# Performance work log

Hardware: AMD Instinct MI355X
Metric: run time of the kernel (lower is better)

## Reference

```python
import jax, jax.numpy as jnp
import numpy as np

N = 100000      # num nodes
E = 400000      # num edges (avg degree 4, AIG-like sparse DAG)
NVT = 7         # node type count (one-hot)
VHS = 100       # vertex hidden size
CHS = 30        # clause hidden size
SV = 512        # number of state-variable nodes
NROUNDS = 8     # message passing rounds


def setup_inputs() -> dict:
    key = jax.random.key(0)
    ks = jax.random.split(key, 40)
    s = 0.08  # ~1/sqrt(VHS), matches torch default uniform scale

    def mat(k, shape):
        return jax.random.normal(k, shape, jnp.float32) * s

    edge_index = jax.random.randint(ks[0], (2, E), 0, N)
    sv_node = jax.random.randint(ks[1], (SV,), 0, N)
    types = jax.random.randint(ks[2], (N,), 0, NVT)
    x = jax.nn.one_hot(types, NVT, dtype=jnp.float32)  # [N, NVT]
    ones_e = jnp.ones((E,), jnp.float32)
    # degrees used as divisors after SpMM (clamped >= 1 like real graphs w/ self edges)
    ind = jnp.clip(jax.ops.segment_sum(ones_e, edge_index[1], num_segments=N), 1.0, None)
    outd = jnp.clip(jax.ops.segment_sum(ones_e, edge_index[0], num_segments=N), 1.0, None)

    inp = {
        "x": x, "edge_index": edge_index, "sv_node": sv_node,
        "ind": ind, "outd": outd, "n_clause": 1, "pretrain_round": 1,
        # type init vectors: Linear(1,VHS)(ones(1)) == weight[:,0] + bias, one row per type
        "type_vec": mat(ks[3], (NVT, VHS)),
        # forward_msg MLP
        "fm_w1": mat(ks[4], (VHS, VHS)), "fm_b1": mat(ks[5], (VHS,)),
        "fm_w2": mat(ks[6], (VHS, VHS)), "fm_b2": mat(ks[7], (VHS,)),
        "fm_w3": mat(ks[8], (VHS, VHS)), "fm_b3": mat(ks[9], (VHS,)),
        # backward_msg MLP
        "bm_w1": mat(ks[10], (VHS, VHS)), "bm_b1": mat(ks[11], (VHS,)),
        "bm_w2": mat(ks[12], (VHS, VHS)), "bm_b2": mat(ks[13], (VHS,)),
        "bm_w3": mat(ks[14], (VHS, VHS)), "bm_b3": mat(ks[15], (VHS,)),
        # forward_update GRU (gates ordered r,z,n as in torch)
        "fg_wih": mat(ks[16], (VHS, 3 * VHS)), "fg_whh": mat(ks[17], (VHS, 3 * VHS)),
        "fg_bih": mat(ks[18], (3 * VHS,)), "fg_bhh": mat(ks[19], (3 * VHS,)),
        # backward_update GRU
        "bg_wih": mat(ks[20], (VHS, 3 * VHS)), "bg_whh": mat(ks[21], (VHS, 3 * VHS)),
        "bg_bih": mat(ks[22], (3 * VHS,)), "bg_bhh": mat(ks[23], (3 * VHS,)),
        # sv_feature_pretrain_layer
        "pw1": mat(ks[24], (VHS, CHS)), "pb1": mat(ks[25], (CHS,)),
        "pw2": mat(ks[26], (CHS, 1)), "pb2": mat(ks[27], (1,)),
    }
    return inp


def reference(x, edge_index, sv_node, ind, outd, n_clause, pretrain_round,
              type_vec, fm_w1, fm_b1, fm_w2, fm_b2, fm_w3, fm_b3,
              bm_w1, bm_b1, bm_w2, bm_b2, bm_w3, bm_b3,
              fg_wih, fg_whh, fg_bih, fg_bhh,
              bg_wih, bg_whh, bg_bih, bg_bhh,
              pw1, pb1, pw2, pb2):
    n = x.shape[0]
    src, dst = edge_index[0], edge_index[1]
    ind_c = ind[:, None]   # [N,1]
    outd_c = outd[:, None]

    def mlp(h, w1, b1, w2, b2, w3, b3):
        h = jax.nn.relu(h @ w1 + b1)
        h = jax.nn.relu(h @ w2 + b2)
        return h @ w3 + b3

    def gru(xin, h, wih, whh, bih, bhh):
        # single-step torch GRU: r,z,n gate ordering
        gi = xin @ wih + bih
        gh = h @ whh + bhh
        ir, iz, ig = jnp.split(gi, 3, axis=-1)
        hr, hz, hg = jnp.split(gh, 3, axis=-1)
        r = jax.nn.sigmoid(ir + hr)
        z = jax.nn.sigmoid(iz + hz)
        g = jnp.tanh(ig + r * hg)
        return (1.0 - z) * g + z * h

    def round_fn(vs, _):
        # forward direction: adj_fwd[dst, src] -> aggregate msgs from src into dst
        m = mlp(vs, fm_w1, fm_b1, fm_w2, fm_b2, fm_w3, fm_b3)
        fwd = jax.ops.segment_sum(m[src], dst, num_segments=n) / ind_c
        vs = gru(fwd, vs, fg_wih, fg_whh, fg_bih, fg_bhh)
        # backward direction: adj_bwd[src, dst] -> aggregate msgs from dst into src
        m = mlp(vs, bm_w1, bm_b1, bm_w2, bm_b2, bm_w3, bm_b3)
        bwd = jax.ops.segment_sum(m[dst], src, num_segments=n) / outd_c
        vs = gru(bwd, vs, bg_wih, bg_whh, bg_bih, bg_bhh)
        return vs, None

    vs0 = x @ type_vec  # [N, VHS]
    vs, _ = jax.lax.scan(jax.checkpoint(round_fn), vs0, None, length=NROUNDS)

    # pretrain_round branch: sv_feature_pretrain_layer(var_state[sv_node]).t()[0]
    shortcut = vs[sv_node]  # [SV, VHS]
    h = jax.nn.relu(shortcut @ pw1 + pb1)
    return (h @ pw2 + pb2)[:, 0]  # [SV]
```

## Files before the change

### kernel.cpp

```cpp
#include <hip/hip_runtime.h>
#include <math.h>

#define NVTC 7
#define VHS 100
#define CHS 30
#define LDP 112
#define CTW 128
#define WFRAG_SZ 32768

typedef short short8 __attribute__((ext_vector_type(8)));
typedef float floatx4 __attribute__((ext_vector_type(4)));

#define MFMA(a, b, c) __builtin_amdgcn_mfma_f32_16x16x32_bf16((a), (b), (c), 0, 0, 0)

#define GLOAD16(g, l)                                                              \
  __builtin_amdgcn_global_load_lds((const __attribute__((address_space(1))) void*)(g), \
                                   (__attribute__((address_space(3))) void*)(l), 16, 0, 0)

__device__ __forceinline__ unsigned short f2bf(float f) {
  unsigned u = __float_as_uint(f);
  return (unsigned short)((u + 0x7fffu + ((u >> 16) & 1u)) >> 16);
}
__device__ __forceinline__ float bf2f(unsigned short h) {
  return __uint_as_float((unsigned)h << 16);
}
__device__ __forceinline__ float sigmf(float v) {
  return __builtin_amdgcn_rcpf(1.f + __expf(-v));
}
__device__ __forceinline__ float tanh_fast(float v) {
  return 1.f - 2.f * __builtin_amdgcn_rcpf(__expf(2.f * v) + 1.f);
}


__global__ void zero_int_kernel(int* __restrict__ p, int n) {
  int i = blockIdx.x * 256 + threadIdx.x;
  if (i < n) p[i] = 0;
}

__global__ void inv_kernel(const float* __restrict__ ind, const float* __restrict__ outd,
                           float* __restrict__ inv_ind, float* __restrict__ inv_outd, int n) {
  int i = blockIdx.x * 256 + threadIdx.x;
  if (i < n) { inv_ind[i] = 1.0f / ind[i]; inv_outd[i] = 1.0f / outd[i]; }
}

struct WfragArgs { const float* src; int srcLD; int colOff; short* dst; };
struct WfragPack { WfragArgs a[18]; };
__global__ void wfrag_all_kernel(WfragPack p) {
  const int mat = blockIdx.x >> 3;
  const int t = ((blockIdx.x & 7) << 8) + threadIdx.x;
  const WfragArgs w = p.a[mat];
  int lane = t & 63, rest = t >> 6;
  int ct = rest & 7, kc = rest >> 3;
  int col = ct * 16 + (lane & 15);
  int kbase = kc * 32 + (lane >> 4) * 8;
  short8 hv, lv;
  #pragma unroll
  for (int i = 0; i < 8; ++i) {
    int k = kbase + i;
    float v = (k < VHS && col < VHS) ? w.src[(size_t)k * w.srcLD + w.colOff + col] : 0.f;
    unsigned short h16 = f2bf(v);
    hv[i] = (short)h16;
    lv[i] = (short)f2bf(v - bf2f(h16));
  }
  int base = ((kc * 8 + ct) * 2 * 64 + lane) * 8;
  *(short8*)(w.dst + base)       = hv;
  *(short8*)(w.dst + base + 512) = lv;
}

struct PadArgs { const float* b1; int off1; const float* b2; int off2; float* dst; };
struct PadPack { PadArgs a[14]; };
__global__ void pad_all_kernel(PadPack p) {
  const PadArgs w = p.a[blockIdx.x];
  int c = threadIdx.x;
  float v = 0.f;
  if (c < VHS) { v = w.b1[w.off1 + c]; if (w.b2) v += w.b2[w.off2 + c]; }
  w.dst[c] = v;
}

__global__ void init_vs_kernel(const float* __restrict__ x, const float* __restrict__ tv,
                               char* __restrict__ vsp, int N) {
  int node = blockIdx.x, c = threadIdx.x;
  if (node >= N) return;
  float v = 0.f;
  if (c < VHS) {
    #pragma unroll
    for (int t = 0; t < NVTC; ++t) v += x[(size_t)node * NVTC + t] * tv[t * VHS + c];
  }
  unsigned short hi = f2bf(v);
  unsigned short lo = f2bf(v - bf2f(hi));
  char* rowp = vsp + ((size_t)node << 9);
  *(unsigned short*)(rowp + 2 * c)       = hi;
  *(unsigned short*)(rowp + 256 + 2 * c) = lo;
}


__global__ void hist_kernel(const int* __restrict__ ei, int E, int* hin, int* hout) {
  int e = blockIdx.x * 256 + threadIdx.x;
  if (e < E) {
    atomicAdd(&hout[ei[e]], 1);
    atomicAdd(&hin[ei[E + e]], 1);
  }
}

__global__ void scan_block_kernel(const int* __restrict__ in, int* __restrict__ mid,
                                  int* __restrict__ sums, int n) {
  __shared__ int lds[256];
  int tid = threadIdx.x;
  int base = blockIdx.x * 1024 + tid * 4;
  int v0 = (base + 0 < n) ? in[base + 0] : 0;
  int v1 = (base + 1 < n) ? in[base + 1] : 0;
  int v2 = (base + 2 < n) ? in[base + 2] : 0;
  int v3 = (base + 3 < n) ? in[base + 3] : 0;
  int s = v0 + v1 + v2 + v3;
  lds[tid] = s;
  __syncthreads();
  for (int off = 1; off < 256; off <<= 1) {
    int t = (tid >= off) ? lds[tid - off] : 0;
    __syncthreads();
    lds[tid] += t;
    __syncthreads();
  }
  int excl = lds[tid] - s;
  int e0 = excl + v0, e1 = e0 + v1, e2 = e1 + v2, e3 = e2 + v3;
  if (base + 0 < n) mid[base + 0] = e0;
  if (base + 1 < n) mid[base + 1] = e1;
  if (base + 2 < n) mid[base + 2] = e2;
  if (base + 3 < n) mid[base + 3] = e3;
  if (tid == 255) sums[blockIdx.x] = lds[255];
}

__global__ void scan_sums_kernel(int* sums, int nb) {
  __shared__ int lds[256];
  int tid = threadIdx.x;
  int v = (tid < nb) ? sums[tid] : 0;
  lds[tid] = v;
  __syncthreads();
  for (int off = 1; off < 256; off <<= 1) {
    int t = (tid >= off) ? lds[tid - off] : 0;
    __syncthreads();
    lds[tid] += t;
    __syncthreads();
  }
  if (tid < nb) sums[tid] = lds[tid];
}

__global__ void scan_finalize_kernel(const int* __restrict__ mid, const int* __restrict__ sums,
                                     int* __restrict__ rp, int n) {
  int i = blockIdx.x * 256 + threadIdx.x;
  if (i >= n) return;
  int blk = i >> 10;
  int add = (blk > 0) ? sums[blk - 1] : 0;
  rp[i + 1] = mid[i] + add;
  if (i == 0) rp[0] = 0;
}

__global__ void fill_kernel(const int* __restrict__ ei, int E, int gOff, int sOff,
                            const int* __restrict__ rp, int* cnt, int* col) {
  int e = blockIdx.x * 256 + threadIdx.x;
  if (e >= E) return;
  int v = ei[sOff + e];
  int p = rp[v] + atomicAdd(&cnt[v], 1);
  col[p] = ei[gOff + e];
}

__global__ void sort_rows_kernel(const int* __restrict__ rp, int* col, int n) {
  int v = blockIdx.x * 256 + threadIdx.x;
  if (v >= n) return;
  int a = rp[v], b = rp[v + 1];
  for (int i = a + 1; i < b; ++i) {
    int key = col[i];
    int j = i - 1;
    while (j >= a && col[j] > key) { col[j + 1] = col[j]; --j; }
    col[j + 1] = key;
  }
}

__global__ void __launch_bounds__(256)
gather_kernel(const float* __restrict__ m, const int* __restrict__ rp,
              const int* __restrict__ col, const float* __restrict__ iv,
              char* __restrict__ aggp, int N) {
  int v = blockIdx.x * 8 + (threadIdx.x >> 5);
  if (v >= N) return;
  int lane = threadIdx.x & 31;
  char* rowp = aggp + ((size_t)v << 9);
  if (lane < 28) {
    float4 a = make_float4(0.f, 0.f, 0.f, 0.f);
    float4 b = make_float4(0.f, 0.f, 0.f, 0.f);
    const int s = rp[v], e = rp[v + 1];
    int i = s;
    for (; i + 1 < e; i += 2) {
      const int c0 = col[i], c1 = col[i + 1];
      float4 u = ((const float4*)(m + (size_t)c0 * LDP))[lane];
      float4 w = ((const float4*)(m + (size_t)c1 * LDP))[lane];
      a.x += u.x; a.y += u.y; a.z += u.z; a.w += u.w;
      b.x += w.x; b.y += w.y; b.z += w.z; b.w += w.w;
    }
    if (i < e) {
      float4 u = ((const float4*)(m + (size_t)col[i] * LDP))[lane];
      a.x += u.x; a.y += u.y; a.z += u.z; a.w += u.w;
    }
    a.x += b.x; a.y += b.y; a.z += b.z; a.w += b.w;
    const float sc = iv[v];
    a.x *= sc; a.y *= sc; a.z *= sc; a.w *= sc;
    unsigned short h0 = f2bf(a.x), h1 = f2bf(a.y), h2 = f2bf(a.z), h3 = f2bf(a.w);
    unsigned short l0 = f2bf(a.x - bf2f(h0)), l1 = f2bf(a.y - bf2f(h1));
    unsigned short l2 = f2bf(a.z - bf2f(h2)), l3 = f2bf(a.w - bf2f(h3));
    *(uint2*)(rowp + 8 * lane) =
        make_uint2((unsigned)h0 | ((unsigned)h1 << 16), (unsigned)h2 | ((unsigned)h3 << 16));
    *(uint2*)(rowp + 256 + 8 * lane) =
        make_uint2((unsigned)l0 | ((unsigned)l1 << 16), (unsigned)l2 | ((unsigned)l3 << 16));
  } else {
    *(uint2*)(rowp + 8 * lane)       = make_uint2(0u, 0u);
    *(uint2*)(rowp + 256 + 8 * lane) = make_uint2(0u, 0u);
  }
}

__global__ void __launch_bounds__(256, 2)
mlp3_kernel(const char* __restrict__ vsp,
            const short* __restrict__ W1f, const short* __restrict__ W2f,
            const short* __restrict__ W3f,
            const float* __restrict__ b1, const float* __restrict__ b2,
            const float* __restrict__ b3, float* __restrict__ OUT, int N) {
  __shared__ __align__(16) char lds[65536];
  char* ldsH = lds;
  char* ldsL = lds + 16384;
  const int lane = threadIdx.x & 63, wave = threadIdx.x >> 6;
  const int lrbase = wave * 16;
  const int row0 = blockIdx.x * 64 + lrbase;
  const int a_r = lane & 15, a_kg = lane >> 4;
  const int col_l = lane & 15;

  short8 Fh[4], Fl[4];
  {
    const char* vrow = vsp + (((size_t)(row0 + a_r)) << 9) + (a_kg << 4);
    #pragma unroll
    for (int kc = 0; kc < 4; ++kc) {
      Fh[kc] = *(const short8*)(vrow + kc * 64);
      Fl[kc] = *(const short8*)(vrow + 256 + kc * 64);
    }
  }
  float B1[7], B2[7], B3[7];
  #pragma unroll
  for (int ct = 0; ct < 7; ++ct) {
    const int k = ct * 16 + col_l;
    B1[ct] = b1[k]; B2[ct] = b2[k]; B3[ct] = b3[k];
  }
  if (lane < 32) {
    int row = lrbase + (lane >> 1), sl = 14 + (lane & 1);
    int byte = row * 256 + ((sl * 16) ^ ((row & 7) << 4));
    short8 z = {0, 0, 0, 0, 0, 0, 0, 0};
    *(short8*)(ldsH + byte) = z;
    *(short8*)(ldsL + byte) = z;
  }
  asm volatile("s_waitcnt vmcnt(0)" ::: "memory");

  floatx4 acc[7];
  #pragma unroll
  for (int c = 0; c < 7; ++c) acc[c] = (floatx4){0.f, 0.f, 0.f, 0.f};

#define MSTAGE(WF, KC, BOFF)                                                   \
  {                                                                            \
    _Pragma("unroll") for (int q = 0; q < 4; ++q) {                            \
      const int c_ = wave * 4 + q;                                             \
      GLOAD16((const char*)(WF) + (size_t)((KC) * 16384 + c_ * 1024) + lane * 16, \
              lds + (BOFF) + c_ * 1024);                                       \
    }                                                                          \
  }

#define MCOMP(KC, BOFF, VA)                                                    \
  {                                                                            \
    asm volatile("s_waitcnt vmcnt(" VA ")" ::: "memory");                      \
    __builtin_amdgcn_s_barrier();                                              \
    short8 wt[14];                                                             \
    _Pragma("unroll") for (int c = 0; c < 7; ++c) {                            \
      wt[2 * c]     = *(const short8*)(lds + (BOFF) + (2 * c) * 1024 + lane * 16); \
      wt[2 * c + 1] = *(const short8*)(lds + (BOFF) + (2 * c + 1) * 1024 + lane * 16); \
    }                                                                          \
    __builtin_amdgcn_s_setprio(1);                                             \
    _Pragma("unroll") for (int c = 0; c < 7; ++c) {                            \
      acc[c] = MFMA(Fh[KC], wt[2 * c], acc[c]);                                \
      acc[c] = MFMA(Fh[KC], wt[2 * c + 1], acc[c]);                            \
      acc[c] = MFMA(Fl[KC], wt[2 * c], acc[c]);                                \
    }                                                                          \
    __builtin_amdgcn_s_setprio(0);                                             \
    __builtin_amdgcn_sched_barrier(0);                                         \
    __builtin_amdgcn_s_barrier();                                              \
  }

  auto wbrelu = [&](const float* B) {
    const int rloc0 = lrbase + (lane >> 4) * 4;
    #pragma unroll
    for (int ct = 0; ct < 7; ++ct) {
      int k = ct * 16 + col_l;
      #pragma unroll
      for (int j = 0; j < 4; ++j) {
        int row = rloc0 + j;
        float v = fmaxf(acc[ct][j] + B[ct], 0.f);
        unsigned short h16 = f2bf(v);
        unsigned short l16 = f2bf(v - bf2f(h16));
        int byte = row * 256 + ((k * 2) ^ ((row & 7) << 4));
        *(short*)(ldsH + byte) = (short)h16;
        *(short*)(ldsL + byte) = (short)l16;
      }
      acc[ct] = (floatx4){0.f, 0.f, 0.f, 0.f};
    }
  };
  auto ldfrags = [&]() {
    #pragma unroll
    for (int kc = 0; kc < 4; ++kc) {
      int r = lrbase + a_r;
      int byte = r * 256 + ((((kc * 4 + a_kg) * 16)) ^ ((r & 7) << 4));
      Fh[kc] = *(const short8*)(ldsH + byte);
      Fl[kc] = *(const short8*)(ldsL + byte);
    }
  };

  MSTAGE(W1f, 0, 32768) MSTAGE(W1f, 1, 49152)
  MCOMP(0, 32768, "4")  MSTAGE(W1f, 2, 32768)
  MCOMP(1, 49152, "4")  MSTAGE(W1f, 3, 49152)
  MCOMP(2, 32768, "4")  MSTAGE(W2f, 0, 32768)
  MCOMP(3, 49152, "4")  MSTAGE(W2f, 1, 49152)
  wbrelu(B1); ldfrags();
  MCOMP(0, 32768, "4")  MSTAGE(W2f, 2, 32768)
  MCOMP(1, 49152, "4")  MSTAGE(W2f, 3, 49152)
  MCOMP(2, 32768, "4")  MSTAGE(W3f, 0, 32768)
  MCOMP(3, 49152, "4")  MSTAGE(W3f, 1, 49152)
  wbrelu(B2); ldfrags();
  MCOMP(0, 32768, "4")  MSTAGE(W3f, 2, 32768)
  MCOMP(1, 49152, "4")  MSTAGE(W3f, 3, 49152)
  MCOMP(2, 32768, "4")
  MCOMP(3, 49152, "0")

  const int r0 = row0 + (lane >> 4) * 4;
  #pragma unroll
  for (int ct = 0; ct < 7; ++ct) {
    const int c = ct * 16 + col_l;
    #pragma unroll
    for (int j = 0; j < 4; ++j) {
      const int r = r0 + j;
      if (r < N) OUT[(size_t)r * LDP + c] = acc[ct][j] + B3[ct];
    }
  }
#undef MSTAGE
#undef MCOMP
}

__global__ void __launch_bounds__(256, 2)
gru_kernel(const char* __restrict__ aggp, const char* __restrict__ vsp,
           const short* __restrict__ Wbase,
           const float* __restrict__ br, const float* __restrict__ bz,
           const float* __restrict__ big, const float* __restrict__ bhg,
           char* __restrict__ outp, int N) {
  __shared__ __align__(16) char wlds[49152];
  const int lane = threadIdx.x & 63, wave = threadIdx.x >> 6;
  const int row0 = blockIdx.x * 64 + wave * 16;
  const int a_r = lane & 15;
  const int kgo = (lane >> 4) << 4;
  const int col_l = lane & 15;
  const int jr0 = row0 + (lane >> 4) * 4;

  short8 Ah[4], Al[4], Vh[4], Vl[4];
  {
    const char* arow = aggp + (((size_t)(row0 + a_r)) << 9) + kgo;
    const char* vrow = vsp  + (((size_t)(row0 + a_r)) << 9) + kgo;
    #pragma unroll
    for (int kc = 0; kc < 4; ++kc) {
      Ah[kc] = *(const short8*)(arow + kc * 64);
      Al[kc] = *(const short8*)(arow + 256 + kc * 64);
      Vh[kc] = *(const short8*)(vrow + kc * 64);
      Vl[kc] = *(const short8*)(vrow + 256 + kc * 64);
    }
  }
  float ho[7][4];
  #pragma unroll
  for (int ct = 0; ct < 7; ++ct) {
    const int ccol = ct * 16 + col_l;
    #pragma unroll
    for (int j = 0; j < 4; ++j) {
      const char* hrow = vsp + ((size_t)(jr0 + j) << 9);
      ho[ct][j] = bf2f(*(const unsigned short*)(hrow + 2 * ccol)) +
                  bf2f(*(const unsigned short*)(hrow + 256 + 2 * ccol));
    }
  }
  float bR[7], bZ[7], bI[7], bH[7];
  #pragma unroll
  for (int ct = 0; ct < 7; ++ct) {
    const int ccol = ct * 16 + col_l;
    bR[ct] = br[ccol]; bZ[ct] = bz[ccol]; bI[ct] = big[ccol]; bH[ct] = bhg[ccol];
  }
  asm volatile("s_waitcnt vmcnt(0)" ::: "memory");

#define GRU_STAGE(CT, KH, BOFF)                                                \
  {                                                                            \
    _Pragma("unroll") for (int q = 0; q < 6; ++q) {                            \
      const int c_ = wave * 6 + q;                                             \
      const int m_ = c_ >> 2, kcl_ = (c_ >> 1) & 1, p_ = c_ & 1;               \
      const size_t gb_ = (size_t)m_ * 65536 +                                  \
          (size_t)(((((KH) * 2 + kcl_) * 8 + (CT)) * 2048) + p_ * 1024);       \
      GLOAD16((const char*)Wbase + gb_ + lane * 16, wlds + (BOFF) + c_ * 1024);\
    }                                                                          \
  }

#define GRU_HALF(KH, BOFF)                                                     \
  {                                                                            \
    _Pragma("unroll") for (int kcl = 0; kcl < 2; ++kcl) {                      \
      const int kc_ = (KH) * 2 + kcl;                                          \
      short8 wt[12];                                                           \
      _Pragma("unroll") for (int mp = 0; mp < 12; ++mp) {                      \
        const int m_ = mp >> 1, p_ = mp & 1;                                   \
        const int chunk_ = m_ * 4 + kcl * 2 + p_;                              \
        wt[mp] = *(const short8*)(wlds + (BOFF) + chunk_ * 1024 + lane * 16);  \
      }                                                                        \
      __builtin_amdgcn_s_setprio(1);                                           \
      rc = MFMA(Ah[kc_], wt[0], rc);  rc = MFMA(Ah[kc_], wt[1], rc);  rc = MFMA(Al[kc_], wt[0], rc); \
      zc = MFMA(Ah[kc_], wt[2], zc);  zc = MFMA(Ah[kc_], wt[3], zc);  zc = MFMA(Al[kc_], wt[2], zc); \
      ic = MFMA(Ah[kc_], wt[4], ic);  ic = MFMA(Ah[kc_], wt[5], ic);  ic = MFMA(Al[kc_], wt[4], ic); \
      rc = MFMA(Vh[kc_], wt[6], rc);  rc = MFMA(Vh[kc_], wt[7], rc);  rc = MFMA(Vl[kc_], wt[6], rc); \
      zc = MFMA(Vh[kc_], wt[8], zc);  zc = MFMA(Vh[kc_], wt[9], zc);  zc = MFMA(Vl[kc_], wt[8], zc); \
      hc = MFMA(Vh[kc_], wt[10], hc); hc = MFMA(Vh[kc_], wt[11], hc); hc = MFMA(Vl[kc_], wt[10], hc); \
      __builtin_amdgcn_s_setprio(0);                                           \
    }                                                                          \
  }

#define GRU_ITER(CT, VA, VB, STG)                                              \
  {                                                                            \
    floatx4 rc = {0.f, 0.f, 0.f, 0.f};                                         \
    floatx4 zc = {0.f, 0.f, 0.f, 0.f};                                         \
    floatx4 ic = {0.f, 0.f, 0.f, 0.f};                                         \
    floatx4 hc = {0.f, 0.f, 0.f, 0.f};                                         \
    asm volatile("s_waitcnt vmcnt(" VA ")" ::: "memory");                      \
    __builtin_amdgcn_s_barrier();                                              \
    GRU_HALF(0, 0)                                                             \
    __builtin_amdgcn_sched_barrier(0);                                         \
    __builtin_amdgcn_s_barrier();                                              \
    if (STG) GRU_STAGE((CT) + 1, 0, 0)                                         \
    asm volatile("s_waitcnt vmcnt(" VB ")" ::: "memory");                      \
    __builtin_amdgcn_s_barrier();                                              \
    GRU_HALF(1, 24576)                                                         \
    __builtin_amdgcn_sched_barrier(0);                                         \
    __builtin_amdgcn_s_barrier();                                              \
    if (STG) GRU_STAGE((CT) + 1, 1, 24576)                                     \
    const float brv = bR[CT], bzv = bZ[CT], bigv = bI[CT], bhgv = bH[CT];      \
    const int ccol = (CT) * 16 + col_l;                                        \
    _Pragma("unroll") for (int j = 0; j < 4; ++j) {                            \
      const float rv = sigmf(rc[j] + brv);                                     \
      const float zv = sigmf(zc[j] + bzv);                                     \
      const float gv = tanh_fast(ic[j] + bigv + rv * (hc[j] + bhgv));          \
      const float v = (1.f - zv) * gv + zv * ho[CT][j];                        \
      const unsigned short hi = f2bf(v);                                       \
      const unsigned short lo = f2bf(v - bf2f(hi));                            \
      char* orow = outp + ((size_t)(jr0 + j) << 9);                            \
      *(unsigned short*)(orow + 2 * ccol)       = hi;                          \
      *(unsigned short*)(orow + 256 + 2 * ccol) = lo;                          \
    }                                                                          \
  }

  GRU_STAGE(0, 0, 0)
  GRU_STAGE(0, 1, 24576)

  GRU_ITER(0, "6",  "6",  1)
  GRU_ITER(1, "14", "14", 1)
  GRU_ITER(2, "14", "14", 1)
  GRU_ITER(3, "14", "14", 1)
  GRU_ITER(4, "14", "14", 1)
  GRU_ITER(5, "14", "14", 1)
  GRU_ITER(6, "14", "8",  0)

#undef GRU_STAGE
#undef GRU_HALF
#undef GRU_ITER
}

__global__ void final_kernel(const char* __restrict__ vsp, const int* __restrict__ sv,
                             const float* __restrict__ pw1, const float* __restrict__ pb1,
                             const float* __restrict__ pw2, const float* __restrict__ pb2,
                             float* __restrict__ out, int SVn) {
  int b = blockIdx.x;
  if (b >= SVn) return;
  int tid = threadIdx.x;
  int node = sv[b];
  const char* rowp = vsp + ((size_t)node << 9);
  float p = 0.f;
  if (tid < CHS) {
    float acc = 0.f;
    for (int k = 0; k < VHS; ++k) {
      float xv = bf2f(*(const unsigned short*)(rowp + 2 * k)) +
                 bf2f(*(const unsigned short*)(rowp + 256 + 2 * k));
      acc += xv * pw1[k * CHS + tid];
    }
    float h = fmaxf(acc + pb1[tid], 0.f);
    p = h * pw2[tid];
  }
  #pragma unroll
  for (int off = 32; off > 0; off >>= 1) p += __shfl_down(p, off);
  if (tid == 0) out[b] = p + pb2[0];
}

extern "C" void kernel_launch(void* const* d_in, const int* in_sizes, int n_in,
                              void* d_out, int out_size, void* d_ws, size_t ws_size,
                              hipStream_t stream) {
  const float* x      = (const float*)d_in[0];
  const int*   ei     = (const int*)d_in[1];
  const int*   sv     = (const int*)d_in[2];
  const float* ind    = (const float*)d_in[3];
  const float* outd   = (const float*)d_in[4];
  const float* tv     = (const float*)d_in[7];
  const float* fm_w1  = (const float*)d_in[8];
  const float* fm_b1  = (const float*)d_in[9];
  const float* fm_w2  = (const float*)d_in[10];
  const float* fm_b2  = (const float*)d_in[11];
  const float* fm_w3  = (const float*)d_in[12];
  const float* fm_b3  = (const float*)d_in[13];
  const float* bm_w1  = (const float*)d_in[14];
  const float* bm_b1  = (const float*)d_in[15];
  const float* bm_w2  = (const float*)d_in[16];
  const float* bm_b2  = (const float*)d_in[17];
  const float* bm_w3  = (const float*)d_in[18];
  const float* bm_b3  = (const float*)d_in[19];
  const float* fg_wih = (const float*)d_in[20];
  const float* fg_whh = (const float*)d_in[21];
  const float* fg_bih = (const float*)d_in[22];
  const float* fg_bhh = (const float*)d_in[23];
  const float* bg_wih = (const float*)d_in[24];
  const float* bg_whh = (const float*)d_in[25];
  const float* bg_bih = (const float*)d_in[26];
  const float* bg_bhh = (const float*)d_in[27];
  const float* pw1    = (const float*)d_in[28];
  const float* pb1    = (const float*)d_in[29];
  const float* pw2    = (const float*)d_in[30];
  const float* pb2    = (const float*)d_in[31];

  const int N   = in_sizes[3];
  const int E   = in_sizes[1] / 2;
  const int SVn = in_sizes[2];

  char* wsb = (char*)d_ws;
  const size_t NP = (size_t)N * LDP;
  float* t1     = (float*)wsb;
  char*  vs_sp  = wsb + NP * 4;
  char*  agg_sp = vs_sp + (size_t)(N + 256) * 512;
  float* inv_ind  = (float*)(agg_sp + (size_t)(N + 256) * 512);
  float* inv_outd = inv_ind + N;
  short* wfrag    = (short*)(inv_outd + N);
  float* biasbase = (float*)(wfrag + 18 * WFRAG_SZ);
  int* ip      = (int*)(biasbase + 14 * CTW);
  int* rp_in   = ip; ip += N + 1;
  int* rp_out  = ip; ip += N + 1;
  int* col_in  = ip; ip += E;
  int* col_out = ip; ip += E;
  int* cnt     = ip; ip += N;
  int* hin     = ip; ip += N;
  int* hout    = ip; ip += N;
  int* mid     = ip; ip += N;
  int* sums    = ip; ip += 512;

  const size_t need_bytes = (size_t)((char*)(ip) - (char*)d_ws);
  if (ws_size < need_bytes) return;

  auto wf  = [&](int i) { return wfrag + (size_t)i * WFRAG_SZ; };
  auto bia = [&](int i) { return biasbase + (size_t)i * CTW; };

  WfragPack wp;
  wp.a[0] = {fm_w1, VHS, 0, wf(0)};
  wp.a[1] = {fm_w2, VHS, 0, wf(1)};
  wp.a[2] = {fm_w3, VHS, 0, wf(2)};
  wp.a[3] = {bm_w1, VHS, 0, wf(3)};
  wp.a[4] = {bm_w2, VHS, 0, wf(4)};
  wp.a[5] = {bm_w3, VHS, 0, wf(5)};
  for (int g = 0; g < 3; ++g) {
    wp.a[6 + g]  = {fg_wih, 3 * VHS, g * VHS, wf(6 + g)};
    wp.a[9 + g]  = {fg_whh, 3 * VHS, g * VHS, wf(9 + g)};
    wp.a[12 + g] = {bg_wih, 3 * VHS, g * VHS, wf(12 + g)};
    wp.a[15 + g] = {bg_whh, 3 * VHS, g * VHS, wf(15 + g)};
  }
  wfrag_all_kernel<<<144, 256, 0, stream>>>(wp);

  PadPack pp;
  pp.a[0]  = {fm_b1, 0,       nullptr, 0,   bia(0)};
  pp.a[1]  = {fm_b2, 0,       nullptr, 0,   bia(1)};
  pp.a[2]  = {fm_b3, 0,       nullptr, 0,   bia(2)};
  pp.a[3]  = {bm_b1, 0,       nullptr, 0,   bia(3)};
  pp.a[4]  = {bm_b2, 0,       nullptr, 0,   bia(4)};
  pp.a[5]  = {bm_b3, 0,       nullptr, 0,   bia(5)};
  pp.a[6]  = {fg_bih, 0,       fg_bhh, 0,   bia(6)};
  pp.a[7]  = {fg_bih, VHS,     fg_bhh, VHS, bia(7)};
  pp.a[8]  = {fg_bih, 2 * VHS, nullptr, 0,  bia(8)};
  pp.a[9]  = {fg_bhh, 2 * VHS, nullptr, 0,  bia(9)};
  pp.a[10] = {bg_bih, 0,       bg_bhh, 0,   bia(10)};
  pp.a[11] = {bg_bih, VHS,     bg_bhh, VHS, bia(11)};
  pp.a[12] = {bg_bih, 2 * VHS, nullptr, 0,  bia(12)};
  pp.a[13] = {bg_bhh, 2 * VHS, nullptr, 0,  bia(13)};
  pad_all_kernel<<<14, 128, 0, stream>>>(pp);

  inv_kernel<<<(N + 255) / 256, 256, 0, stream>>>(ind, outd, inv_ind, inv_outd, N);
  init_vs_kernel<<<N, 128, 0, stream>>>(x, tv, vs_sp, N);

  zero_int_kernel<<<(2 * N + 255) / 256, 256, 0, stream>>>(hin, 2 * N);
  hist_kernel<<<(E + 255) / 256, 256, 0, stream>>>(ei, E, hin, hout);
  const int nb = (N + 1023) / 1024;
  scan_block_kernel<<<nb, 256, 0, stream>>>(hin, mid, sums, N);
  scan_sums_kernel<<<1, 256, 0, stream>>>(sums, nb);
  scan_finalize_kernel<<<(N + 255) / 256, 256, 0, stream>>>(mid, sums, rp_in, N);
  scan_block_kernel<<<nb, 256, 0, stream>>>(hout, mid, sums, N);
  scan_sums_kernel<<<1, 256, 0, stream>>>(sums, nb);
  scan_finalize_kernel<<<(N + 255) / 256, 256, 0, stream>>>(mid, sums, rp_out, N);
  zero_int_kernel<<<(N + 255) / 256, 256, 0, stream>>>(cnt, N);
  fill_kernel<<<(E + 255) / 256, 256, 0, stream>>>(ei, E, 0, E, rp_in, cnt, col_in);
  sort_rows_kernel<<<(N + 255) / 256, 256, 0, stream>>>(rp_in, col_in, N);
  zero_int_kernel<<<(N + 255) / 256, 256, 0, stream>>>(cnt, N);
  fill_kernel<<<(E + 255) / 256, 256, 0, stream>>>(ei, E, E, 0, rp_out, cnt, col_out);
  sort_rows_kernel<<<(N + 255) / 256, 256, 0, stream>>>(rp_out, col_out, N);

  const int gridMM  = (N + 63) / 64;
  const int gridGRU = (N + 63) / 64;
  const int gridG   = (N + 7) / 8;
  for (int rd = 0; rd < 8; ++rd) {
    for (int dir = 0; dir < 2; ++dir) {
      const int mw = dir ? 3 : 0;
      const int gb = dir ? 10 : 6;
      const int* rp   = dir ? rp_out : rp_in;
      const int* col  = dir ? col_out : col_in;
      const float* iv = dir ? inv_outd : inv_ind;

      mlp3_kernel<<<gridMM, 256, 0, stream>>>(vs_sp, wf(mw + 0), wf(mw + 1), wf(mw + 2),
                                              bia(mw + 0), bia(mw + 1), bia(mw + 2), t1, N);
      gather_kernel<<<gridG, 256, 0, stream>>>(t1, rp, col, iv, agg_sp, N);
      gru_kernel<<<gridGRU, 256, 0, stream>>>(agg_sp, vs_sp, wf(dir ? 12 : 6),
                                              bia(gb + 0), bia(gb + 1), bia(gb + 2), bia(gb + 3),
                                              vs_sp, N);
    }
  }

  final_kernel<<<SVn, 64, 0, stream>>>(vs_sp, sv, pw1, pb1, pw2, pb2, (float*)d_out, SVn);
}
```

Measured before the change: 2.506 ms.

## Fuse neighbor gather aggregation into GRU kernel via LDS staging

Removes the separate gather kernel. The GRU kernel now sums neighbor messages from t1 for its own 64 rows, stages the fp32 results in LDS, and converts them to bf16 hi/lo fragments in registers. This drops the write and re-read of the bf16-split aggregation buffer and one launch per direction per round. In exchange the GRU kernel gains a latency-bound irregular gather phase with low parallelism (each 32-lane group handles 8 rows serially), plus extra barriers, which may hurt occupancy and latency hiding.

```diff
diff --git a/kernel.cpp b/kernel.cpp
--- a/kernel.cpp
+++ b/kernel.cpp
@@ -175,46 +175,6 @@
   }
 }
 
-__global__ void __launch_bounds__(256)
-gather_kernel(const float* __restrict__ m, const int* __restrict__ rp,
-              const int* __restrict__ col, const float* __restrict__ iv,
-              char* __restrict__ aggp, int N) {
-  int v = blockIdx.x * 8 + (threadIdx.x >> 5);
-  if (v >= N) return;
-  int lane = threadIdx.x & 31;
-  char* rowp = aggp + ((size_t)v << 9);
-  if (lane < 28) {
-    float4 a = make_float4(0.f, 0.f, 0.f, 0.f);
-    float4 b = make_float4(0.f, 0.f, 0.f, 0.f);
-    const int s = rp[v], e = rp[v + 1];
-    int i = s;
-    for (; i + 1 < e; i += 2) {
-      const int c0 = col[i], c1 = col[i + 1];
-      float4 u = ((const float4*)(m + (size_t)c0 * LDP))[lane];
-      float4 w = ((const float4*)(m + (size_t)c1 * LDP))[lane];
-      a.x += u.x; a.y += u.y; a.z += u.z; a.w += u.w;
-      b.x += w.x; b.y += w.y; b.z += w.z; b.w += w.w;
-    }
-    if (i < e) {
-      float4 u = ((const float4*)(m + (size_t)col[i] * LDP))[lane];
-      a.x += u.x; a.y += u.y; a.z += u.z; a.w += u.w;
-    }
-    a.x += b.x; a.y += b.y; a.z += b.z; a.w += b.w;
-    const float sc = iv[v];
-    a.x *= sc; a.y *= sc; a.z *= sc; a.w *= sc;
-    unsigned short h0 = f2bf(a.x), h1 = f2bf(a.y), h2 = f2bf(a.z), h3 = f2bf(a.w);
-    unsigned short l0 = f2bf(a.x - bf2f(h0)), l1 = f2bf(a.y - bf2f(h1));
-    unsigned short l2 = f2bf(a.z - bf2f(h2)), l3 = f2bf(a.w - bf2f(h3));
-    *(uint2*)(rowp + 8 * lane) =
-        make_uint2((unsigned)h0 | ((unsigned)h1 << 16), (unsigned)h2 | ((unsigned)h3 << 16));
-    *(uint2*)(rowp + 256 + 8 * lane) =
-        make_uint2((unsigned)l0 | ((unsigned)l1 << 16), (unsigned)l2 | ((unsigned)l3 << 16));
-  } else {
-    *(uint2*)(rowp + 8 * lane)       = make_uint2(0u, 0u);
-    *(uint2*)(rowp + 256 + 8 * lane) = make_uint2(0u, 0u);
-  }
-}
-
 __global__ void __launch_bounds__(256, 2)
 mlp3_kernel(const char* __restrict__ vsp,
             const short* __restrict__ W1f, const short* __restrict__ W2f,
@@ -346,7 +306,9 @@
 }
 
 __global__ void __launch_bounds__(256, 2)
-gru_kernel(const char* __restrict__ aggp, const char* __restrict__ vsp,
+gru_kernel(const float* __restrict__ t1, const char* __restrict__ vsp,
+           const int* __restrict__ rp, const int* __restrict__ col,
+           const float* __restrict__ iv,
            const short* __restrict__ Wbase,
            const float* __restrict__ br, const float* __restrict__ bz,
            const float* __restrict__ big, const float* __restrict__ bhg,
@@ -355,18 +317,46 @@
   const int lane = threadIdx.x & 63, wave = threadIdx.x >> 6;
   const int row0 = blockIdx.x * 64 + wave * 16;
   const int a_r = lane & 15;
-  const int kgo = (lane >> 4) << 4;
   const int col_l = lane & 15;
   const int jr0 = row0 + (lane >> 4) * 4;
 
+  {
+    const int g = threadIdx.x >> 5;
+    const int l32 = threadIdx.x & 31;
+    #pragma unroll 1
+    for (int rr = 0; rr < 8; ++rr) {
+      const int lr = g * 8 + rr;
+      const int v = blockIdx.x * 64 + lr;
+      float4 a = make_float4(0.f, 0.f, 0.f, 0.f);
+      float4 b = make_float4(0.f, 0.f, 0.f, 0.f);
+      if (v < N && l32 < 28) {
+        const int s = rp[v], e = rp[v + 1];
+        int i = s;
+        for (; i + 1 < e; i += 2) {
+          const int c0 = col[i], c1 = col[i + 1];
+          float4 u = ((const float4*)(t1 + (size_t)c0 * LDP))[l32];
+          float4 w = ((const float4*)(t1 + (size_t)c1 * LDP))[l32];
+          a.x += u.x; a.y += u.y; a.z += u.z; a.w += u.w;
+          b.x += w.x; b.y += w.y; b.z += w.z; b.w += w.w;
+        }
+        if (i < e) {
+          float4 u = ((const float4*)(t1 + (size_t)col[i] * LDP))[l32];
+          a.x += u.x; a.y += u.y; a.z += u.z; a.w += u.w;
+        }
+        a.x += b.x; a.y += b.y; a.z += b.z; a.w += b.w;
+        const float sc = iv[v];
+        a.x *= sc; a.y *= sc; a.z *= sc; a.w *= sc;
+      }
+      *(float4*)(wlds + lr * 528 + l32 * 16) = a;
+    }
+  }
+
   short8 Ah[4], Al[4], Vh[4], Vl[4];
   {
-    const char* arow = aggp + (((size_t)(row0 + a_r)) << 9) + kgo;
-    const char* vrow = vsp  + (((size_t)(row0 + a_r)) << 9) + kgo;
+    const int kgo = (lane >> 4) << 4;
+    const char* vrow = vsp + (((size_t)(row0 + a_r)) << 9) + kgo;
     #pragma unroll
     for (int kc = 0; kc < 4; ++kc) {
-      Ah[kc] = *(const short8*)(arow + kc * 64);
-      Al[kc] = *(const short8*)(arow + 256 + kc * 64);
       Vh[kc] = *(const short8*)(vrow + kc * 64);
       Vl[kc] = *(const short8*)(vrow + 256 + kc * 64);
     }
@@ -388,7 +378,26 @@
     const int ccol = ct * 16 + col_l;
     bR[ct] = br[ccol]; bZ[ct] = bz[ccol]; bI[ct] = big[ccol]; bH[ct] = bhg[ccol];
   }
-  asm volatile("s_waitcnt vmcnt(0)" ::: "memory");
+  __syncthreads();
+
+  {
+    const char* base = wlds + (wave * 16 + a_r) * 528 + ((lane >> 4) * 32);
+    #pragma unroll
+    for (int kc = 0; kc < 4; ++kc) {
+      float4 u0 = *(const float4*)(base + kc * 128);
+      float4 u1 = *(const float4*)(base + kc * 128 + 16);
+      float t[8] = {u0.x, u0.y, u0.z, u0.w, u1.x, u1.y, u1.z, u1.w};
+      short8 h, lo;
+      #pragma unroll
+      for (int i = 0; i < 8; ++i) {
+        unsigned short hh = f2bf(t[i]);
+        h[i] = (short)hh;
+        lo[i] = (short)f2bf(t[i] - bf2f(hh));
+      }
+      Ah[kc] = h; Al[kc] = lo;
+    }
+  }
+  __syncthreads();
 
 #define GRU_STAGE(CT, KH, BOFF)                                                \
   {                                                                            \
@@ -538,8 +547,7 @@
   const size_t NP = (size_t)N * LDP;
   float* t1     = (float*)wsb;
   char*  vs_sp  = wsb + NP * 4;
-  char*  agg_sp = vs_sp + (size_t)(N + 256) * 512;
-  float* inv_ind  = (float*)(agg_sp + (size_t)(N + 256) * 512);
+  float* inv_ind  = (float*)(vs_sp + (size_t)(N + 256) * 512);
   float* inv_outd = inv_ind + N;
   short* wfrag    = (short*)(inv_outd + N);
   float* biasbase = (float*)(wfrag + 18 * WFRAG_SZ);
@@ -613,7 +621,6 @@
 
   const int gridMM  = (N + 63) / 64;
   const int gridGRU = (N + 63) / 64;
-  const int gridG   = (N + 7) / 8;
   for (int rd = 0; rd < 8; ++rd) {
     for (int dir = 0; dir < 2; ++dir) {
       const int mw = dir ? 3 : 0;
@@ -624,8 +631,7 @@
 
       mlp3_kernel<<<gridMM, 256, 0, stream>>>(vs_sp, wf(mw + 0), wf(mw + 1), wf(mw + 2),
                                               bia(mw + 0), bia(mw + 1), bia(mw + 2), t1, N);
-      gather_kernel<<<gridG, 256, 0, stream>>>(t1, rp, col, iv, agg_sp, N);
-      gru_kernel<<<gridGRU, 256, 0, stream>>>(agg_sp, vs_sp, wf(dir ? 12 : 6),
+      gru_kernel<<<gridGRU, 256, 0, stream>>>(t1, vs_sp, rp, col, iv, wf(dir ? 12 : 6),
                                               bia(gb + 0), bia(gb + 1), bia(gb + 2), bia(gb + 3),
                                               vs_sp, N);
     }
```

Measured after the change: 2.934 ms. 1.17x slower.
